# Kernel tuning notes

Measured on AMD Instinct MI355X. Metric: run time of the kernel, lower is better.

Reference implementation:

```python
import jax, jax.numpy as jnp
import numpy as np

N_NODES = 50000
N_EDGES = 800000
N_FEAT = 256
HIDDEN = 64
N_CLASSES = 16
T_END = 3.0  # opt['time']; rk4 takes one step over [0, 3]


def spline_conv(x, src, dst, p, W, R, b, n):
    """SplineConv, dim=1, kernel_size=2, degree=1 open B-spline, aggr='mean'.
    x: [n, Cin]; src/dst: [E]; p: [E,1] pseudo-coords in [0,1];
    W: [2, Cin, Cout]; R: [Cin, Cout]; b: [Cout]."""
    xj = x[src]  # gather source node features [E, Cin]
    # basis weights for K=2, degree=1: (1-p) on kernel 0, p on kernel 1
    msg = ((1.0 - p) * xj) @ W[0] + (p * xj) @ W[1]  # [E, Cout]
    agg = jax.ops.segment_sum(msg, dst, num_segments=n)
    deg = jax.ops.segment_sum(jnp.ones((msg.shape[0], 1), msg.dtype), dst, num_segments=n)
    return agg / jnp.maximum(deg, 1.0) + x @ R + b


def setup_inputs() -> dict:
    key = jax.random.key(0)
    ks = jax.random.split(key, 20)
    x = jax.random.normal(ks[0], (N_NODES, N_FEAT), jnp.float32)
    edge_attr = jax.random.uniform(ks[1], (N_EDGES, 1), jnp.float32)
    src = jax.random.randint(ks[2], (N_EDGES,), 0, N_NODES)
    dst = jax.random.randint(ks[3], (N_EDGES,), 0, N_NODES)

    def w(k, shape, fan_in):
        s = 1.0 / np.sqrt(fan_in)
        return jax.random.uniform(k, shape, jnp.float32, -s, s)

    # conv1: num_features -> hidden
    W1 = w(ks[4], (2, N_FEAT, HIDDEN), N_FEAT)
    R1 = w(ks[5], (N_FEAT, HIDDEN), N_FEAT)
    b1 = jnp.zeros((HIDDEN,), jnp.float32)
    # ODE func: two stacked SplineConvs hidden -> hidden
    Wa = w(ks[6], (2, HIDDEN, HIDDEN), HIDDEN)
    Ra = w(ks[7], (HIDDEN, HIDDEN), HIDDEN)
    ba = jnp.zeros((HIDDEN,), jnp.float32)
    Wb = w(ks[8], (2, HIDDEN, HIDDEN), HIDDEN)
    Rb = w(ks[9], (HIDDEN, HIDDEN), HIDDEN)
    bb = jnp.zeros((HIDDEN,), jnp.float32)
    # conv2: hidden -> num_classes
    W2 = w(ks[10], (2, HIDDEN, N_CLASSES), HIDDEN)
    R2 = w(ks[11], (HIDDEN, N_CLASSES), HIDDEN)
    b2 = jnp.zeros((N_CLASSES,), jnp.float32)

    return dict(x=x, edge_attr=edge_attr, src=src, dst=dst,
                W1=W1, R1=R1, b1=b1, Wa=Wa, Ra=Ra, ba=ba,
                Wb=Wb, Rb=Rb, bb=bb, W2=W2, R2=R2, b2=b2)


def reference(x, edge_attr, src, dst, W1, R1, b1, Wa, Ra, ba, Wb, Rb, bb, W2, R2, b2):
    n = x.shape[0]
    p = edge_attr
    h = jnp.tanh(spline_conv(x, src, dst, p, W1, R1, b1, n))
    # dropout is identity in eval mode

    def f(y):  # GCNLayer: two stacked SplineConvs, no activation
        y = spline_conv(y, src, dst, p, Wa, Ra, ba, n)
        return spline_conv(y, src, dst, p, Wb, Rb, bb, n)

    # single RK4 step from t=0 to t=T_END (torchdiffeq fixed-grid rk4 on s_span=[0,3])
    k1 = f(h)
    k2 = f(h + 0.5 * T_END * k1)
    k3 = f(h + 0.5 * T_END * k2)
    k4 = f(h + T_END * k3)
    h = h + (T_END / 6.0) * (k1 + 2.0 * k2 + 2.0 * k3 + k4)

    out = jnp.tanh(spline_conv(h, src, dst, p, W2, R2, b2, n))
    return jax.nn.log_softmax(out, axis=1)
```

## Files before the change

### kernel.cpp

```cpp
#include <hip/hip_runtime.h>
#include <math.h>

static inline int ceil_div(int a, int b) { return (a + b - 1) / b; }


__global__ __launch_bounds__(256) void zero2(int* __restrict__ a, int* __restrict__ b,
                                             int n) {
    int i = blockIdx.x * 256 + threadIdx.x;
    if (i < n) { a[i] = 0; b[i] = 0; }
}

__global__ __launch_bounds__(256) void hist_kernel(const int* __restrict__ dst,
                                                   int* __restrict__ deg, int E) {
    int e = blockIdx.x * 256 + threadIdx.x;
    if (e < E) atomicAdd(&deg[dst[e]], 1);
}

__global__ __launch_bounds__(256) void scan_blocksum(const int* __restrict__ deg,
                                                     int* __restrict__ bsum, int n) {
    __shared__ int red[256];
    int t = threadIdx.x;
    int base = blockIdx.x * 2048 + t * 8;
    int s = 0;
    #pragma unroll
    for (int i = 0; i < 8; ++i) {
        int idx = base + i;
        if (idx < n) s += deg[idx];
    }
    red[t] = s;
    __syncthreads();
    #pragma unroll
    for (int off = 128; off >= 1; off >>= 1) {
        if (t < off) red[t] += red[t + off];
        __syncthreads();
    }
    if (t == 0) bsum[blockIdx.x] = red[0];
}

__global__ __launch_bounds__(256) void scan_tops(int* __restrict__ bsum, int nb) {
    __shared__ int sh[256];
    int t = threadIdx.x;
    int orig = (t < nb) ? bsum[t] : 0;
    sh[t] = orig;
    __syncthreads();
    for (int off = 1; off < 256; off <<= 1) {
        int add = (t >= off) ? sh[t - off] : 0;
        __syncthreads();
        sh[t] += add;
        __syncthreads();
    }
    if (t < nb) bsum[t] = sh[t] - orig;
}

__global__ __launch_bounds__(256) void scan_final(const int* __restrict__ deg,
                                                  const int* __restrict__ bsum,
                                                  int* __restrict__ rowp,
                                                  float* __restrict__ invd,
                                                  int n, int E) {
    __shared__ int sh[256];
    int t = threadIdx.x;
    int base = blockIdx.x * 2048 + t * 8;
    int loc[8];
    int s = 0;
    #pragma unroll
    for (int i = 0; i < 8; ++i) {
        int idx = base + i;
        int d = (idx < n) ? deg[idx] : 0;
        loc[i] = d;
        s += d;
    }
    sh[t] = s;
    __syncthreads();
    for (int off = 1; off < 256; off <<= 1) {
        int add = (t >= off) ? sh[t - off] : 0;
        __syncthreads();
        sh[t] += add;
        __syncthreads();
    }
    int run = bsum[blockIdx.x] + (sh[t] - s);
    #pragma unroll
    for (int i = 0; i < 8; ++i) {
        int idx = base + i;
        if (idx < n) {
            rowp[idx] = run;
            int d = loc[i];
            run += d;
            invd[idx] = 1.0f / (float)(d > 1 ? d : 1);
        }
    }
    if (blockIdx.x == 0 && t == 0) rowp[n] = E;
}

__global__ __launch_bounds__(256) void scatter_idx(const int* __restrict__ dst,
                                                   const int* __restrict__ rowp,
                                                   int* __restrict__ fill,
                                                   int* __restrict__ ei, int E) {
    int e = blockIdx.x * 256 + threadIdx.x;
    if (e >= E) return;
    int d = dst[e];
    int pos = rowp[d] + atomicAdd(&fill[d], 1);
    ei[pos] = e;
}

__global__ __launch_bounds__(256) void sort_fill(const int* __restrict__ rowp,
                                                 int* __restrict__ ei,
                                                 const int* __restrict__ src,
                                                 const float* __restrict__ p,
                                                 int* __restrict__ es,
                                                 float* __restrict__ ep, int n) {
    int node = blockIdx.x * 256 + threadIdx.x;
    if (node >= n) return;
    int b = rowp[node], e = rowp[node + 1];
    for (int i = b + 1; i < e; ++i) {
        int key = ei[i];
        int j = i - 1;
        while (j >= b && ei[j] > key) { ei[j + 1] = ei[j]; --j; }
        ei[j + 1] = key;
    }
    for (int i = b; i < e; ++i) {
        int id = ei[i];
        es[i] = src[id];
        ep[i] = p[id];
    }
}

__global__ __launch_bounds__(256) void pack_all(
    const float* __restrict__ W1, const float* __restrict__ R1,
    const float* __restrict__ Wa, const float* __restrict__ Ra,
    const float* __restrict__ Wb, const float* __restrict__ Rb,
    const float* __restrict__ W2, const float* __restrict__ R2,
    float* __restrict__ Bc1, float* __restrict__ Bca,
    float* __restrict__ Bcb, float* __restrict__ Bc2) {
    int idx = blockIdx.x * 256 + threadIdx.x;
    const int S1 = 256 * 192, S2 = 192 * 64, S4 = 64 * 48;
    if (idx < S1) {
        int k = idx / 192, c = idx % 192;
        float v;
        if (c < 64)       v = W1[k * 64 + c];
        else if (c < 128) v = W1[256 * 64 + k * 64 + (c - 64)];
        else              v = R1[k * 64 + (c - 128)];
        Bc1[idx] = v;
        return;
    }
    idx -= S1;
    if (idx < S2) { Bca[idx] = (idx < 8192) ? Wa[idx] : Ra[idx - 8192]; return; }
    idx -= S2;
    if (idx < S2) { Bcb[idx] = (idx < 8192) ? Wb[idx] : Rb[idx - 8192]; return; }
    idx -= S2;
    if (idx < S4) {
        int k = idx / 48, c = idx % 48;
        float v;
        if (c < 16)      v = W2[k * 16 + c];
        else if (c < 32) v = W2[64 * 16 + k * 16 + (c - 16)];
        else             v = R2[k * 16 + (c - 32)];
        Bc2[idx] = v;
    }
}

__global__ __launch_bounds__(256) void edge_agg64_v4(const float* __restrict__ x,
                                                     const int* __restrict__ rowp,
                                                     const int* __restrict__ es,
                                                     const float* __restrict__ ep,
                                                     const float* __restrict__ invd,
                                                     float* __restrict__ agg, int n) {
    int gid = blockIdx.x * 256 + threadIdx.x;
    int node = gid >> 4;
    if (node >= n) return;
    int c4 = (gid & 15) << 2;
    int e = rowp[node], eend = rowp[node + 1];
    float sx = 0.f, sy = 0.f, sz = 0.f, sw = 0.f;
    float px = 0.f, py = 0.f, pz = 0.f, pw = 0.f;
    for (; e + 4 <= eend; e += 4) {
        int s0 = es[e], s1 = es[e + 1], s2 = es[e + 2], s3 = es[e + 3];
        float p0 = ep[e], p1 = ep[e + 1], p2 = ep[e + 2], p3 = ep[e + 3];
        float4 v0 = *reinterpret_cast<const float4*>(&x[(size_t)s0 * 64 + c4]);
        float4 v1 = *reinterpret_cast<const float4*>(&x[(size_t)s1 * 64 + c4]);
        float4 v2 = *reinterpret_cast<const float4*>(&x[(size_t)s2 * 64 + c4]);
        float4 v3 = *reinterpret_cast<const float4*>(&x[(size_t)s3 * 64 + c4]);
        sx += (v0.x + v1.x) + (v2.x + v3.x);
        sy += (v0.y + v1.y) + (v2.y + v3.y);
        sz += (v0.z + v1.z) + (v2.z + v3.z);
        sw += (v0.w + v1.w) + (v2.w + v3.w);
        px = fmaf(p0, v0.x, fmaf(p1, v1.x, fmaf(p2, v2.x, fmaf(p3, v3.x, px))));
        py = fmaf(p0, v0.y, fmaf(p1, v1.y, fmaf(p2, v2.y, fmaf(p3, v3.y, py))));
        pz = fmaf(p0, v0.z, fmaf(p1, v1.z, fmaf(p2, v2.z, fmaf(p3, v3.z, pz))));
        pw = fmaf(p0, v0.w, fmaf(p1, v1.w, fmaf(p2, v2.w, fmaf(p3, v3.w, pw))));
    }
    for (; e < eend; ++e) {
        int s = es[e];
        float pe = ep[e];
        float4 v = *reinterpret_cast<const float4*>(&x[(size_t)s * 64 + c4]);
        sx += v.x; sy += v.y; sz += v.z; sw += v.w;
        px = fmaf(pe, v.x, px); py = fmaf(pe, v.y, py);
        pz = fmaf(pe, v.z, pz); pw = fmaf(pe, v.w, pw);
    }
    float w = invd[node];
    float4 a0 = make_float4((sx - px) * w, (sy - py) * w, (sz - pz) * w, (sw - pw) * w);
    float4 a1 = make_float4(px * w, py * w, pz * w, pw * w);
    *reinterpret_cast<float4*>(&agg[(size_t)node * 128 + c4]) = a0;
    *reinterpret_cast<float4*>(&agg[(size_t)node * 128 + 64 + c4]) = a1;
}

__global__ __launch_bounds__(256) void hidden_gemm_db(
    const float* __restrict__ agg, const float* __restrict__ in,
    const float* __restrict__ B, const float* __restrict__ bias,
    int n, int mode, float* __restrict__ u_out,
    const float* __restrict__ hbuf, const float* __restrict__ acc_in,
    float* __restrict__ acc_out, float* __restrict__ t_out,
    float c1, float c2, float c3) {
    __shared__ __align__(16) float As[2][16][68];
    __shared__ __align__(16) float Bs[2][16][68];
    const int t = threadIdx.x;
    const int row0 = blockIdx.x * 64;
    const int ty = t >> 4, tx = t & 15;
    const int lrow = t >> 2, lk = (t & 3) << 2;
    const int bkk = t >> 4, bcol = (t & 15) << 2;

    float4 av = make_float4(0.f, 0.f, 0.f, 0.f);
    {
        int r = row0 + lrow;
        if (r < n) av = *reinterpret_cast<const float4*>(&agg[(size_t)r * 128 + lk]);
    }
    float4 bv = *reinterpret_cast<const float4*>(&B[(size_t)bkk * 64 + bcol]);
    As[0][lk + 0][lrow] = av.x; As[0][lk + 1][lrow] = av.y;
    As[0][lk + 2][lrow] = av.z; As[0][lk + 3][lrow] = av.w;
    *reinterpret_cast<float4*>(&Bs[0][bkk][bcol]) = bv;
    __syncthreads();

    float acc[4][4];
    #pragma unroll
    for (int i = 0; i < 4; ++i)
        #pragma unroll
        for (int j = 0; j < 4; ++j) acc[i][j] = 0.f;

    for (int kt = 0; kt < 12; ++kt) {
        const int cur = kt & 1;
        if (kt + 1 < 12) {
            int k0 = (kt + 1) << 4;
            int r = row0 + lrow;
            int kk = k0 + lk;
            av = make_float4(0.f, 0.f, 0.f, 0.f);
            if (r < n)
                av = (kk < 128)
                    ? *reinterpret_cast<const float4*>(&agg[(size_t)r * 128 + kk])
                    : *reinterpret_cast<const float4*>(&in[(size_t)r * 64 + (kk - 128)]);
            bv = *reinterpret_cast<const float4*>(&B[(size_t)(k0 + bkk) * 64 + bcol]);
        }
        #pragma unroll
        for (int kk = 0; kk < 16; ++kk) {
            float4 a4 = *reinterpret_cast<const float4*>(&As[cur][kk][ty << 2]);
            float4 b4 = *reinterpret_cast<const float4*>(&Bs[cur][kk][tx << 2]);
            float aa[4] = {a4.x, a4.y, a4.z, a4.w};
            float bb[4] = {b4.x, b4.y, b4.z, b4.w};
            #pragma unroll
            for (int i = 0; i < 4; ++i)
                #pragma unroll
                for (int j = 0; j < 4; ++j)
                    acc[i][j] = fmaf(aa[i], bb[j], acc[i][j]);
        }
        if (kt + 1 < 12) {
            const int nx = cur ^ 1;
            As[nx][lk + 0][lrow] = av.x; As[nx][lk + 1][lrow] = av.y;
            As[nx][lk + 2][lrow] = av.z; As[nx][lk + 3][lrow] = av.w;
            *reinterpret_cast<float4*>(&Bs[nx][bkk][bcol]) = bv;
        }
        __syncthreads();
    }

    float4 bia = *reinterpret_cast<const float4*>(&bias[tx << 2]);
    #pragma unroll
    for (int i = 0; i < 4; ++i) {
        int r = row0 + (ty << 2) + i;
        if (r >= n) continue;
        size_t idx = (size_t)r * 64 + (tx << 2);
        float4 v = make_float4(acc[i][0] + bia.x, acc[i][1] + bia.y,
                               acc[i][2] + bia.z, acc[i][3] + bia.w);
        if (mode == 0) {
            *reinterpret_cast<float4*>(&u_out[idx]) = v;
        } else {
            float4 ai = make_float4(0.f, 0.f, 0.f, 0.f);
            if (acc_in) ai = *reinterpret_cast<const float4*>(&acc_in[idx]);
            float4 an = make_float4(ai.x + c3 * v.x, ai.y + c3 * v.y,
                                    ai.z + c3 * v.z, ai.w + c3 * v.w);
            *reinterpret_cast<float4*>(&acc_out[idx]) = an;
            float4 hb = *reinterpret_cast<const float4*>(&hbuf[idx]);
            float4 to = make_float4(hb.x + c1 * v.x + c2 * an.x,
                                    hb.y + c1 * v.y + c2 * an.y,
                                    hb.z + c1 * v.z + c2 * an.z,
                                    hb.w + c1 * v.w + c2 * an.w);
            *reinterpret_cast<float4*>(&t_out[idx]) = to;
        }
    }
}

__global__ __launch_bounds__(256) void conv1_gemm_db(const float* __restrict__ x,
                                                     const float* __restrict__ B,
                                                     int n, float* __restrict__ yz,
                                                     float* __restrict__ base,
                                                     const float* __restrict__ b1) {
    __shared__ __align__(16) float As[2][16][68];
    __shared__ __align__(16) float Bs[2][16][200];
    const int t = threadIdx.x;
    const int row0 = blockIdx.x * 64;
    const int ty = t >> 4, tx = t & 15;
    const int lrow = t >> 2, lk = (t & 3) << 2;
    const int bkk = t >> 4, bcol = (t & 15) << 2;

    float4 av = make_float4(0.f, 0.f, 0.f, 0.f);
    {
        int r = row0 + lrow;
        if (r < n) av = *reinterpret_cast<const float4*>(&x[(size_t)r * 256 + lk]);
    }
    const float* bp0 = &B[(size_t)bkk * 192 + bcol];
    float4 bv0 = *reinterpret_cast<const float4*>(bp0);
    float4 bv1 = *reinterpret_cast<const float4*>(bp0 + 64);
    float4 bv2 = *reinterpret_cast<const float4*>(bp0 + 128);
    As[0][lk + 0][lrow] = av.x; As[0][lk + 1][lrow] = av.y;
    As[0][lk + 2][lrow] = av.z; As[0][lk + 3][lrow] = av.w;
    *reinterpret_cast<float4*>(&Bs[0][bkk][bcol]) = bv0;
    *reinterpret_cast<float4*>(&Bs[0][bkk][bcol + 64]) = bv1;
    *reinterpret_cast<float4*>(&Bs[0][bkk][bcol + 128]) = bv2;
    __syncthreads();

    float acc[4][12];
    #pragma unroll
    for (int i = 0; i < 4; ++i)
        #pragma unroll
        for (int j = 0; j < 12; ++j) acc[i][j] = 0.f;

    for (int kt = 0; kt < 16; ++kt) {
        const int cur = kt & 1;
        if (kt + 1 < 16) {
            int k0 = (kt + 1) << 4;
            int r = row0 + lrow;
            av = make_float4(0.f, 0.f, 0.f, 0.f);
            if (r < n)
                av = *reinterpret_cast<const float4*>(&x[(size_t)r * 256 + k0 + lk]);
            const float* bp = &B[(size_t)(k0 + bkk) * 192 + bcol];
            bv0 = *reinterpret_cast<const float4*>(bp);
            bv1 = *reinterpret_cast<const float4*>(bp + 64);
            bv2 = *reinterpret_cast<const float4*>(bp + 128);
        }
        #pragma unroll
        for (int kk = 0; kk < 16; ++kk) {
            float4 a4 = *reinterpret_cast<const float4*>(&As[cur][kk][ty << 2]);
            float4 b0 = *reinterpret_cast<const float4*>(&Bs[cur][kk][tx << 2]);
            float4 b1v = *reinterpret_cast<const float4*>(&Bs[cur][kk][(tx << 2) + 64]);
            float4 b2v = *reinterpret_cast<const float4*>(&Bs[cur][kk][(tx << 2) + 128]);
            float aa[4] = {a4.x, a4.y, a4.z, a4.w};
            float bb[12] = {b0.x, b0.y, b0.z, b0.w, b1v.x, b1v.y, b1v.z, b1v.w,
                            b2v.x, b2v.y, b2v.z, b2v.w};
            #pragma unroll
            for (int i = 0; i < 4; ++i)
                #pragma unroll
                for (int j = 0; j < 12; ++j)
                    acc[i][j] = fmaf(aa[i], bb[j], acc[i][j]);
        }
        if (kt + 1 < 16) {
            const int nx = cur ^ 1;
            As[nx][lk + 0][lrow] = av.x; As[nx][lk + 1][lrow] = av.y;
            As[nx][lk + 2][lrow] = av.z; As[nx][lk + 3][lrow] = av.w;
            *reinterpret_cast<float4*>(&Bs[nx][bkk][bcol]) = bv0;
            *reinterpret_cast<float4*>(&Bs[nx][bkk][bcol + 64]) = bv1;
            *reinterpret_cast<float4*>(&Bs[nx][bkk][bcol + 128]) = bv2;
        }
        __syncthreads();
    }

    float4 bb4 = *reinterpret_cast<const float4*>(&b1[tx << 2]);
    #pragma unroll
    for (int i = 0; i < 4; ++i) {
        int r = row0 + (ty << 2) + i;
        if (r >= n) continue;
        float4 q0 = make_float4(acc[i][0], acc[i][1], acc[i][2], acc[i][3]);
        float4 q1 = make_float4(acc[i][4], acc[i][5], acc[i][6], acc[i][7]);
        float4 q2 = make_float4(acc[i][8] + bb4.x, acc[i][9] + bb4.y,
                                acc[i][10] + bb4.z, acc[i][11] + bb4.w);
        *reinterpret_cast<float4*>(&yz[(size_t)r * 128 + (tx << 2)]) = q0;
        *reinterpret_cast<float4*>(&yz[(size_t)r * 128 + 64 + (tx << 2)]) = q1;
        *reinterpret_cast<float4*>(&base[(size_t)r * 64 + (tx << 2)]) = q2;
    }
}


__global__ __launch_bounds__(256) void edge_tf64_v4(const float* __restrict__ yz,
                                                    const int* __restrict__ rowp,
                                                    const int* __restrict__ es,
                                                    const float* __restrict__ ep,
                                                    const float* __restrict__ invd,
                                                    const float* __restrict__ base,
                                                    float* __restrict__ out, int n) {
    int gid = blockIdx.x * 256 + threadIdx.x;
    int node = gid >> 4;
    if (node >= n) return;
    int c4 = (gid & 15) << 2;
    int e = rowp[node], eend = rowp[node + 1];
    float ax = 0.f, ay = 0.f, az = 0.f, aw = 0.f;
    for (; e + 2 <= eend; e += 2) {
        int s0 = es[e], s1 = es[e + 1];
        float p0 = ep[e], p1 = ep[e + 1];
        float4 y0 = *reinterpret_cast<const float4*>(&yz[(size_t)s0 * 128 + c4]);
        float4 z0 = *reinterpret_cast<const float4*>(&yz[(size_t)s0 * 128 + 64 + c4]);
        float4 y1 = *reinterpret_cast<const float4*>(&yz[(size_t)s1 * 128 + c4]);
        float4 z1 = *reinterpret_cast<const float4*>(&yz[(size_t)s1 * 128 + 64 + c4]);
        ax += fmaf(p0, z0.x - y0.x, y0.x) + fmaf(p1, z1.x - y1.x, y1.x);
        ay += fmaf(p0, z0.y - y0.y, y0.y) + fmaf(p1, z1.y - y1.y, y1.y);
        az += fmaf(p0, z0.z - y0.z, y0.z) + fmaf(p1, z1.z - y1.z, y1.z);
        aw += fmaf(p0, z0.w - y0.w, y0.w) + fmaf(p1, z1.w - y1.w, y1.w);
    }
    for (; e < eend; ++e) {
        int s = es[e];
        float pe = ep[e];
        float4 y = *reinterpret_cast<const float4*>(&yz[(size_t)s * 128 + c4]);
        float4 z = *reinterpret_cast<const float4*>(&yz[(size_t)s * 128 + 64 + c4]);
        ax += fmaf(pe, z.x - y.x, y.x);
        ay += fmaf(pe, z.y - y.y, y.y);
        az += fmaf(pe, z.z - y.z, y.z);
        aw += fmaf(pe, z.w - y.w, y.w);
    }
    float w = invd[node];
    size_t idx = (size_t)node * 64 + c4;
    float4 b = *reinterpret_cast<const float4*>(&base[idx]);
    float4 o = make_float4(tanhf(fmaf(ax, w, b.x)), tanhf(fmaf(ay, w, b.y)),
                           tanhf(fmaf(az, w, b.z)), tanhf(fmaf(aw, w, b.w)));
    *reinterpret_cast<float4*>(&out[idx]) = o;
}

__global__ __launch_bounds__(256) void edge_tf16_lsm(const float* __restrict__ yz,
                                                     const int* __restrict__ rowp,
                                                     const int* __restrict__ es,
                                                     const float* __restrict__ ep,
                                                     const float* __restrict__ invd,
                                                     const float* __restrict__ base,
                                                     float* __restrict__ out, int n) {
    int gid = blockIdx.x * 256 + threadIdx.x;
    int node = gid >> 4;
    if (node >= n) return;
    int c = gid & 15;
    int e = rowp[node], eend = rowp[node + 1];
    float a = 0.f;
    for (; e + 4 <= eend; e += 4) {
        int s0 = es[e], s1 = es[e + 1], s2 = es[e + 2], s3 = es[e + 3];
        float p0 = ep[e], p1 = ep[e + 1], p2 = ep[e + 2], p3 = ep[e + 3];
        float y0 = yz[(size_t)s0 * 32 + c],      z0 = yz[(size_t)s0 * 32 + 16 + c];
        float y1 = yz[(size_t)s1 * 32 + c],      z1 = yz[(size_t)s1 * 32 + 16 + c];
        float y2 = yz[(size_t)s2 * 32 + c],      z2 = yz[(size_t)s2 * 32 + 16 + c];
        float y3 = yz[(size_t)s3 * 32 + c],      z3 = yz[(size_t)s3 * 32 + 16 + c];
        a += fmaf(p0, z0 - y0, y0);
        a += fmaf(p1, z1 - y1, y1);
        a += fmaf(p2, z2 - y2, y2);
        a += fmaf(p3, z3 - y3, y3);
    }
    for (; e < eend; ++e) {
        int s = es[e]; float pe = ep[e];
        float y = yz[(size_t)s * 32 + c], z = yz[(size_t)s * 32 + 16 + c];
        a += fmaf(pe, z - y, y);
    }
    float o = tanhf(a * invd[node] + base[(size_t)node * 16 + c]);
    float m = o;
    #pragma unroll
    for (int off = 8; off >= 1; off >>= 1) m = fmaxf(m, __shfl_xor(m, off, 16));
    float ex = expf(o - m);
    float s = ex;
    #pragma unroll
    for (int off = 8; off >= 1; off >>= 1) s += __shfl_xor(s, off, 16);
    out[(size_t)node * 16 + c] = (o - m) - logf(s);
}

__global__ __launch_bounds__(256) void gemm_tiled(
    const float* __restrict__ A0, int lda0, int K0,
    const float* __restrict__ A1, int lda1,
    const float* __restrict__ B,
    int n, int K, int M,
    float* __restrict__ out0, int w0, const float* __restrict__ bias0,
    float* __restrict__ out1, int w1, const float* __restrict__ bias1,
    int split) {
    __shared__ __align__(16) float As[16][68];
    __shared__ __align__(16) float Bs[16][68];
    const int t = threadIdx.x;
    const int row0 = blockIdx.x * 64;
    const int col0 = blockIdx.y * 64;
    const int ty = t >> 4, tx = t & 15;
    const int lrow = t >> 2, lk = (t & 3) << 2;
    const int bkk = t >> 4, bcol = (t & 15) << 2;
    float acc[4][4];
    #pragma unroll
    for (int i = 0; i < 4; ++i)
        #pragma unroll
        for (int j = 0; j < 4; ++j) acc[i][j] = 0.f;

    for (int k0 = 0; k0 < K; k0 += 16) {
        float4 av = make_float4(0.f, 0.f, 0.f, 0.f);
        {
            int r = row0 + lrow;
            if (r < n) {
                int kk = k0 + lk;
                const float* src = (kk < K0)
                    ? (A0 + (size_t)r * lda0 + kk)
                    : (A1 + (size_t)r * lda1 + (kk - K0));
                av = *reinterpret_cast<const float4*>(src);
            }
        }
        float4 bv = make_float4(0.f, 0.f, 0.f, 0.f);
        {
            int c = col0 + bcol;
            int kk = k0 + bkk;
            if (c < M) bv = *reinterpret_cast<const float4*>(B + (size_t)kk * M + c);
        }
        As[lk + 0][lrow] = av.x; As[lk + 1][lrow] = av.y;
        As[lk + 2][lrow] = av.z; As[lk + 3][lrow] = av.w;
        *reinterpret_cast<float4*>(&Bs[bkk][bcol]) = bv;
        __syncthreads();
        #pragma unroll
        for (int kk = 0; kk < 16; ++kk) {
            float4 a4 = *reinterpret_cast<const float4*>(&As[kk][ty << 2]);
            float4 b4 = *reinterpret_cast<const float4*>(&Bs[kk][tx << 2]);
            float aa[4] = {a4.x, a4.y, a4.z, a4.w};
            float bb[4] = {b4.x, b4.y, b4.z, b4.w};
            #pragma unroll
            for (int i = 0; i < 4; ++i)
                #pragma unroll
                for (int j = 0; j < 4; ++j)
                    acc[i][j] = fmaf(aa[i], bb[j], acc[i][j]);
        }
        __syncthreads();
    }

    #pragma unroll
    for (int i = 0; i < 4; ++i) {
        int r = row0 + (ty << 2) + i;
        if (r >= n) continue;
        #pragma unroll
        for (int j = 0; j < 4; ++j) {
            int c = col0 + (tx << 2) + j;
            if (c >= M) continue;
            float v = acc[i][j];
            if (c < split) {
                if (bias0) v += bias0[c];
                out0[(size_t)r * w0 + c] = v;
            } else {
                int cc = c - split;
                if (bias1) v += bias1[cc];
                out1[(size_t)r * w1 + cc] = v;
            }
        }
    }
}


static void hidden_conv(hipStream_t stream, const float* in, float* agg,
                        const int* rowp, const int* es, const float* ep,
                        const float* invd, const float* Bc, const float* bias, int n,
                        int mode, float* u_out,
                        const float* h, const float* acc_in, float* acc_out,
                        float* t_out, float c1, float c2, float c3) {
    edge_agg64_v4<<<ceil_div(n * 16, 256), 256, 0, stream>>>(in, rowp, es, ep, invd,
                                                             agg, n);
    hidden_gemm_db<<<ceil_div(n, 64), 256, 0, stream>>>(agg, in, Bc, bias, n, mode,
                                                        u_out, h, acc_in, acc_out,
                                                        t_out, c1, c2, c3);
}

extern "C" void kernel_launch(void* const* d_in, const int* in_sizes, int n_in,
                              void* d_out, int out_size, void* d_ws, size_t ws_size,
                              hipStream_t stream) {
    const float* x  = (const float*)d_in[0];
    const float* pE = (const float*)d_in[1];
    const int*   sr = (const int*)d_in[2];
    const int*   ds = (const int*)d_in[3];
    const float* W1 = (const float*)d_in[4];
    const float* R1 = (const float*)d_in[5];
    const float* b1 = (const float*)d_in[6];
    const float* Wa = (const float*)d_in[7];
    const float* Ra = (const float*)d_in[8];
    const float* ba = (const float*)d_in[9];
    const float* Wb = (const float*)d_in[10];
    const float* Rb = (const float*)d_in[11];
    const float* bb = (const float*)d_in[12];
    const float* W2 = (const float*)d_in[13];
    const float* R2 = (const float*)d_in[14];
    const float* b2 = (const float*)d_in[15];
    const int n = in_sizes[0] / 256;
    const int E = in_sizes[2];
    float* out = (float*)d_out;

    char* w = (char*)d_ws;
    auto alloc = [&](size_t bytes) -> void* {
        void* ptr = (void*)w;
        w += (bytes + 255) & ~(size_t)255;
        return ptr;
    };
    int nscan = ceil_div(n, 2048);
    int*   deg  = (int*)alloc((size_t)n * 4);
    int*   fill = (int*)alloc((size_t)n * 4);
    int*   rowp = (int*)alloc((size_t)(n + 1) * 4);
    float* invd = (float*)alloc((size_t)n * 4);
    int*   bsum = (int*)alloc((size_t)256 * 4);
    int*   ei   = (int*)alloc((size_t)E * 4);
    int*   es   = (int*)alloc((size_t)E * 4);
    float* ep   = (float*)alloc((size_t)E * 4);
    float* Bc1  = (float*)alloc((size_t)256 * 192 * 4);
    float* Bca  = (float*)alloc((size_t)192 * 64 * 4);
    float* Bcb  = (float*)alloc((size_t)192 * 64 * 4);
    float* Bc2  = (float*)alloc((size_t)64 * 48 * 4);
    float* big0 = (float*)alloc((size_t)n * 128 * 4);
    float* big1 = (float*)alloc((size_t)n * 64 * 4);
    float* h    = (float*)alloc((size_t)n * 64 * 4);
    float* u    = (float*)alloc((size_t)n * 64 * 4);
    float* tb   = (float*)alloc((size_t)n * 64 * 4);
    float* acc  = (float*)alloc((size_t)n * 64 * 4);

    const int PACK_TOTAL = 256 * 192 + 2 * 192 * 64 + 64 * 48;

    zero2<<<ceil_div(n, 256), 256, 0, stream>>>(deg, fill, n);
    pack_all<<<ceil_div(PACK_TOTAL, 256), 256, 0, stream>>>(W1, R1, Wa, Ra, Wb, Rb,
                                                            W2, R2, Bc1, Bca, Bcb, Bc2);
    hist_kernel<<<ceil_div(E, 256), 256, 0, stream>>>(ds, deg, E);
    scan_blocksum<<<nscan, 256, 0, stream>>>(deg, bsum, n);
    scan_tops<<<1, 256, 0, stream>>>(bsum, nscan);
    scan_final<<<nscan, 256, 0, stream>>>(deg, bsum, rowp, invd, n, E);
    scatter_idx<<<ceil_div(E, 256), 256, 0, stream>>>(ds, rowp, fill, ei, E);
    sort_fill<<<ceil_div(n, 256), 256, 0, stream>>>(rowp, ei, sr, pE, es, ep, n);

    const int gb = ceil_div(n, 64);

    conv1_gemm_db<<<gb, 256, 0, stream>>>(x, Bc1, n, big0, big1, b1);
    edge_tf64_v4<<<ceil_div(n * 16, 256), 256, 0, stream>>>(big0, rowp, es, ep, invd,
                                                            big1, h, n);

    hidden_conv(stream, h, big0, rowp, es, ep, invd, Bca, ba, n, 0, u,
                nullptr, nullptr, nullptr, nullptr, 0.f, 0.f, 0.f);
    hidden_conv(stream, u, big0, rowp, es, ep, invd, Bcb, bb, n, 1, nullptr,
                h, nullptr, acc, tb, 1.5f, 0.f, 1.f);
    hidden_conv(stream, tb, big0, rowp, es, ep, invd, Bca, ba, n, 0, u,
                nullptr, nullptr, nullptr, nullptr, 0.f, 0.f, 0.f);
    hidden_conv(stream, u, big0, rowp, es, ep, invd, Bcb, bb, n, 1, nullptr,
                h, acc, acc, tb, 1.5f, 0.f, 2.f);
    hidden_conv(stream, tb, big0, rowp, es, ep, invd, Bca, ba, n, 0, u,
                nullptr, nullptr, nullptr, nullptr, 0.f, 0.f, 0.f);
    hidden_conv(stream, u, big0, rowp, es, ep, invd, Bcb, bb, n, 1, nullptr,
                h, acc, acc, tb, 3.f, 0.f, 2.f);
    hidden_conv(stream, tb, big0, rowp, es, ep, invd, Bca, ba, n, 0, u,
                nullptr, nullptr, nullptr, nullptr, 0.f, 0.f, 0.f);
    hidden_conv(stream, u, big0, rowp, es, ep, invd, Bcb, bb, n, 1, nullptr,
                h, acc, acc, tb, 0.f, 0.5f, 1.f);

    gemm_tiled<<<dim3(gb, 1), 256, 0, stream>>>(tb, 64, 64, nullptr, 0, Bc2, n, 64, 48,
                                                big0, 32, nullptr, big1, 16, b2, 32);
    edge_tf16_lsm<<<ceil_div(n * 16, 256), 256, 0, stream>>>(big0, rowp, es, ep, invd,
                                                             big1, out, n);
}
```

Before: 926.0 us.

## Use 8-channel edge gathers and 32-row single-buffered GEMM tiles

The gather/aggregate kernels now give each thread 8 channels through two float4 loads, so 8 threads cover a node instead of 16. This halves the thread count and the index and weight loads per node, and adds more memory parallelism per thread. The hidden and conv1 GEMMs move from 64-row double-buffered tiles to 32-row single-buffered tiles, doubling the grid for better occupancy and cutting shared memory. The cost is lost load/compute overlap, half the threads idle during A-tile loads, and lower FMA reuse per thread.

```diff
diff --git a/kernel.cpp b/kernel.cpp
--- a/kernel.cpp
+++ b/kernel.cpp
@@ -157,120 +157,125 @@
     }
 }
 
-__global__ __launch_bounds__(256) void edge_agg64_v4(const float* __restrict__ x,
+__global__ __launch_bounds__(256) void edge_agg64_v8(const float* __restrict__ x,
                                                      const int* __restrict__ rowp,
                                                      const int* __restrict__ es,
                                                      const float* __restrict__ ep,
                                                      const float* __restrict__ invd,
                                                      float* __restrict__ agg, int n) {
     int gid = blockIdx.x * 256 + threadIdx.x;
-    int node = gid >> 4;
+    int node = gid >> 3;
     if (node >= n) return;
-    int c4 = (gid & 15) << 2;
+    int c8 = (gid & 7) << 3;
     int e = rowp[node], eend = rowp[node + 1];
-    float sx = 0.f, sy = 0.f, sz = 0.f, sw = 0.f;
-    float px = 0.f, py = 0.f, pz = 0.f, pw = 0.f;
+    float s[8] = {0.f, 0.f, 0.f, 0.f, 0.f, 0.f, 0.f, 0.f};
+    float p[8] = {0.f, 0.f, 0.f, 0.f, 0.f, 0.f, 0.f, 0.f};
     for (; e + 4 <= eend; e += 4) {
-        int s0 = es[e], s1 = es[e + 1], s2 = es[e + 2], s3 = es[e + 3];
+        int n0 = es[e], n1 = es[e + 1], n2 = es[e + 2], n3 = es[e + 3];
         float p0 = ep[e], p1 = ep[e + 1], p2 = ep[e + 2], p3 = ep[e + 3];
-        float4 v0 = *reinterpret_cast<const float4*>(&x[(size_t)s0 * 64 + c4]);
-        float4 v1 = *reinterpret_cast<const float4*>(&x[(size_t)s1 * 64 + c4]);
-        float4 v2 = *reinterpret_cast<const float4*>(&x[(size_t)s2 * 64 + c4]);
-        float4 v3 = *reinterpret_cast<const float4*>(&x[(size_t)s3 * 64 + c4]);
-        sx += (v0.x + v1.x) + (v2.x + v3.x);
-        sy += (v0.y + v1.y) + (v2.y + v3.y);
-        sz += (v0.z + v1.z) + (v2.z + v3.z);
-        sw += (v0.w + v1.w) + (v2.w + v3.w);
-        px = fmaf(p0, v0.x, fmaf(p1, v1.x, fmaf(p2, v2.x, fmaf(p3, v3.x, px))));
-        py = fmaf(p0, v0.y, fmaf(p1, v1.y, fmaf(p2, v2.y, fmaf(p3, v3.y, py))));
-        pz = fmaf(p0, v0.z, fmaf(p1, v1.z, fmaf(p2, v2.z, fmaf(p3, v3.z, pz))));
-        pw = fmaf(p0, v0.w, fmaf(p1, v1.w, fmaf(p2, v2.w, fmaf(p3, v3.w, pw))));
+        float4 v0a = *reinterpret_cast<const float4*>(&x[(size_t)n0 * 64 + c8]);
+        float4 v0b = *reinterpret_cast<const float4*>(&x[(size_t)n0 * 64 + c8 + 4]);
+        float4 v1a = *reinterpret_cast<const float4*>(&x[(size_t)n1 * 64 + c8]);
+        float4 v1b = *reinterpret_cast<const float4*>(&x[(size_t)n1 * 64 + c8 + 4]);
+        float4 v2a = *reinterpret_cast<const float4*>(&x[(size_t)n2 * 64 + c8]);
+        float4 v2b = *reinterpret_cast<const float4*>(&x[(size_t)n2 * 64 + c8 + 4]);
+        float4 v3a = *reinterpret_cast<const float4*>(&x[(size_t)n3 * 64 + c8]);
+        float4 v3b = *reinterpret_cast<const float4*>(&x[(size_t)n3 * 64 + c8 + 4]);
+        const float* f0 = &v0a.x; const float* f1 = &v1a.x;
+        const float* f2 = &v2a.x; const float* f3 = &v3a.x;
+        const float* g0 = &v0b.x; const float* g1 = &v1b.x;
+        const float* g2 = &v2b.x; const float* g3 = &v3b.x;
+        #pragma unroll
+        for (int j = 0; j < 4; ++j) {
+            s[j] += (f0[j] + f1[j]) + (f2[j] + f3[j]);
+            p[j] = fmaf(p0, f0[j], fmaf(p1, f1[j], fmaf(p2, f2[j], fmaf(p3, f3[j], p[j]))));
+        }
+        #pragma unroll
+        for (int j = 0; j < 4; ++j) {
+            s[4 + j] += (g0[j] + g1[j]) + (g2[j] + g3[j]);
+            p[4 + j] = fmaf(p0, g0[j], fmaf(p1, g1[j], fmaf(p2, g2[j], fmaf(p3, g3[j], p[4 + j]))));
+        }
     }
     for (; e < eend; ++e) {
-        int s = es[e];
+        int sn = es[e];
         float pe = ep[e];
-        float4 v = *reinterpret_cast<const float4*>(&x[(size_t)s * 64 + c4]);
-        sx += v.x; sy += v.y; sz += v.z; sw += v.w;
-        px = fmaf(pe, v.x, px); py = fmaf(pe, v.y, py);
-        pz = fmaf(pe, v.z, pz); pw = fmaf(pe, v.w, pw);
+        float4 va = *reinterpret_cast<const float4*>(&x[(size_t)sn * 64 + c8]);
+        float4 vb = *reinterpret_cast<const float4*>(&x[(size_t)sn * 64 + c8 + 4]);
+        const float* fa = &va.x; const float* fb = &vb.x;
+        #pragma unroll
+        for (int j = 0; j < 4; ++j) {
+            s[j] += fa[j];        p[j] = fmaf(pe, fa[j], p[j]);
+            s[4 + j] += fb[j];    p[4 + j] = fmaf(pe, fb[j], p[4 + j]);
+        }
     }
     float w = invd[node];
-    float4 a0 = make_float4((sx - px) * w, (sy - py) * w, (sz - pz) * w, (sw - pw) * w);
-    float4 a1 = make_float4(px * w, py * w, pz * w, pw * w);
-    *reinterpret_cast<float4*>(&agg[(size_t)node * 128 + c4]) = a0;
-    *reinterpret_cast<float4*>(&agg[(size_t)node * 128 + 64 + c4]) = a1;
-}
-
-__global__ __launch_bounds__(256) void hidden_gemm_db(
+    float4 a0, a1, b0, b1v;
+    a0.x = (s[0] - p[0]) * w; a0.y = (s[1] - p[1]) * w;
+    a0.z = (s[2] - p[2]) * w; a0.w = (s[3] - p[3]) * w;
+    a1.x = (s[4] - p[4]) * w; a1.y = (s[5] - p[5]) * w;
+    a1.z = (s[6] - p[6]) * w; a1.w = (s[7] - p[7]) * w;
+    b0.x = p[0] * w; b0.y = p[1] * w; b0.z = p[2] * w; b0.w = p[3] * w;
+    b1v.x = p[4] * w; b1v.y = p[5] * w; b1v.z = p[6] * w; b1v.w = p[7] * w;
+    *reinterpret_cast<float4*>(&agg[(size_t)node * 128 + c8])          = a0;
+    *reinterpret_cast<float4*>(&agg[(size_t)node * 128 + c8 + 4])      = a1;
+    *reinterpret_cast<float4*>(&agg[(size_t)node * 128 + 64 + c8])     = b0;
+    *reinterpret_cast<float4*>(&agg[(size_t)node * 128 + 64 + c8 + 4]) = b1v;
+}
+
+__global__ __launch_bounds__(256) void hidden_gemm32(
     const float* __restrict__ agg, const float* __restrict__ in,
     const float* __restrict__ B, const float* __restrict__ bias,
     int n, int mode, float* __restrict__ u_out,
     const float* __restrict__ hbuf, const float* __restrict__ acc_in,
     float* __restrict__ acc_out, float* __restrict__ t_out,
     float c1, float c2, float c3) {
-    __shared__ __align__(16) float As[2][16][68];
-    __shared__ __align__(16) float Bs[2][16][68];
+    __shared__ __align__(16) float As[16][36];
+    __shared__ __align__(16) float Bs[16][68];
     const int t = threadIdx.x;
-    const int row0 = blockIdx.x * 64;
+    const int row0 = blockIdx.x * 32;
     const int ty = t >> 4, tx = t & 15;
     const int lrow = t >> 2, lk = (t & 3) << 2;
     const int bkk = t >> 4, bcol = (t & 15) << 2;
-
-    float4 av = make_float4(0.f, 0.f, 0.f, 0.f);
-    {
-        int r = row0 + lrow;
-        if (r < n) av = *reinterpret_cast<const float4*>(&agg[(size_t)r * 128 + lk]);
-    }
-    float4 bv = *reinterpret_cast<const float4*>(&B[(size_t)bkk * 64 + bcol]);
-    As[0][lk + 0][lrow] = av.x; As[0][lk + 1][lrow] = av.y;
-    As[0][lk + 2][lrow] = av.z; As[0][lk + 3][lrow] = av.w;
-    *reinterpret_cast<float4*>(&Bs[0][bkk][bcol]) = bv;
-    __syncthreads();
-
-    float acc[4][4];
-    #pragma unroll
-    for (int i = 0; i < 4; ++i)
+    float acc[2][4];
+    #pragma unroll
+    for (int i = 0; i < 2; ++i)
         #pragma unroll
         for (int j = 0; j < 4; ++j) acc[i][j] = 0.f;
 
     for (int kt = 0; kt < 12; ++kt) {
-        const int cur = kt & 1;
-        if (kt + 1 < 12) {
-            int k0 = (kt + 1) << 4;
+        int k0 = kt << 4;
+        if (t < 128) {
             int r = row0 + lrow;
             int kk = k0 + lk;
-            av = make_float4(0.f, 0.f, 0.f, 0.f);
+            float4 av = make_float4(0.f, 0.f, 0.f, 0.f);
             if (r < n)
                 av = (kk < 128)
                     ? *reinterpret_cast<const float4*>(&agg[(size_t)r * 128 + kk])
                     : *reinterpret_cast<const float4*>(&in[(size_t)r * 64 + (kk - 128)]);
-            bv = *reinterpret_cast<const float4*>(&B[(size_t)(k0 + bkk) * 64 + bcol]);
-        }
+            As[lk + 0][lrow] = av.x; As[lk + 1][lrow] = av.y;
+            As[lk + 2][lrow] = av.z; As[lk + 3][lrow] = av.w;
+        }
+        float4 bv = *reinterpret_cast<const float4*>(&B[(size_t)(k0 + bkk) * 64 + bcol]);
+        *reinterpret_cast<float4*>(&Bs[bkk][bcol]) = bv;
+        __syncthreads();
         #pragma unroll
         for (int kk = 0; kk < 16; ++kk) {
-            float4 a4 = *reinterpret_cast<const float4*>(&As[cur][kk][ty << 2]);
-            float4 b4 = *reinterpret_cast<const float4*>(&Bs[cur][kk][tx << 2]);
-            float aa[4] = {a4.x, a4.y, a4.z, a4.w};
+            float a0 = As[kk][ty * 2], a1 = As[kk][ty * 2 + 1];
+            float4 b4 = *reinterpret_cast<const float4*>(&Bs[kk][tx << 2]);
             float bb[4] = {b4.x, b4.y, b4.z, b4.w};
             #pragma unroll
-            for (int i = 0; i < 4; ++i)
-                #pragma unroll
-                for (int j = 0; j < 4; ++j)
-                    acc[i][j] = fmaf(aa[i], bb[j], acc[i][j]);
-        }
-        if (kt + 1 < 12) {
-            const int nx = cur ^ 1;
-            As[nx][lk + 0][lrow] = av.x; As[nx][lk + 1][lrow] = av.y;
-            As[nx][lk + 2][lrow] = av.z; As[nx][lk + 3][lrow] = av.w;
-            *reinterpret_cast<float4*>(&Bs[nx][bkk][bcol]) = bv;
+            for (int j = 0; j < 4; ++j) {
+                acc[0][j] = fmaf(a0, bb[j], acc[0][j]);
+                acc[1][j] = fmaf(a1, bb[j], acc[1][j]);
+            }
         }
         __syncthreads();
     }
 
     float4 bia = *reinterpret_cast<const float4*>(&bias[tx << 2]);
     #pragma unroll
-    for (int i = 0; i < 4; ++i) {
-        int r = row0 + (ty << 2) + i;
+    for (int i = 0; i < 2; ++i) {
+        int r = row0 + ty * 2 + i;
         if (r >= n) continue;
         size_t idx = (size_t)r * 64 + (tx << 2);
         float4 v = make_float4(acc[i][0] + bia.x, acc[i][1] + bia.y,
@@ -293,84 +298,63 @@
     }
 }
 
-__global__ __launch_bounds__(256) void conv1_gemm_db(const float* __restrict__ x,
-                                                     const float* __restrict__ B,
-                                                     int n, float* __restrict__ yz,
-                                                     float* __restrict__ base,
-                                                     const float* __restrict__ b1) {
-    __shared__ __align__(16) float As[2][16][68];
-    __shared__ __align__(16) float Bs[2][16][200];
+__global__ __launch_bounds__(256) void conv1_gemm32(const float* __restrict__ x,
+                                                    const float* __restrict__ B,
+                                                    int n, float* __restrict__ yz,
+                                                    float* __restrict__ base,
+                                                    const float* __restrict__ b1) {
+    __shared__ __align__(16) float As[16][36];
+    __shared__ __align__(16) float Bs[16][200];
     const int t = threadIdx.x;
-    const int row0 = blockIdx.x * 64;
+    const int row0 = blockIdx.x * 32;
     const int ty = t >> 4, tx = t & 15;
     const int lrow = t >> 2, lk = (t & 3) << 2;
     const int bkk = t >> 4, bcol = (t & 15) << 2;
-
-    float4 av = make_float4(0.f, 0.f, 0.f, 0.f);
-    {
-        int r = row0 + lrow;
-        if (r < n) av = *reinterpret_cast<const float4*>(&x[(size_t)r * 256 + lk]);
-    }
-    const float* bp0 = &B[(size_t)bkk * 192 + bcol];
-    float4 bv0 = *reinterpret_cast<const float4*>(bp0);
-    float4 bv1 = *reinterpret_cast<const float4*>(bp0 + 64);
-    float4 bv2 = *reinterpret_cast<const float4*>(bp0 + 128);
-    As[0][lk + 0][lrow] = av.x; As[0][lk + 1][lrow] = av.y;
-    As[0][lk + 2][lrow] = av.z; As[0][lk + 3][lrow] = av.w;
-    *reinterpret_cast<float4*>(&Bs[0][bkk][bcol]) = bv0;
-    *reinterpret_cast<float4*>(&Bs[0][bkk][bcol + 64]) = bv1;
-    *reinterpret_cast<float4*>(&Bs[0][bkk][bcol + 128]) = bv2;
-    __syncthreads();
-
-    float acc[4][12];
-    #pragma unroll
-    for (int i = 0; i < 4; ++i)
+    float acc[2][12];
+    #pragma unroll
+    for (int i = 0; i < 2; ++i)
         #pragma unroll
         for (int j = 0; j < 12; ++j) acc[i][j] = 0.f;
 
     for (int kt = 0; kt < 16; ++kt) {
-        const int cur = kt & 1;
-        if (kt + 1 < 16) {
-            int k0 = (kt + 1) << 4;
+        int k0 = kt << 4;
+        if (t < 128) {
             int r = row0 + lrow;
-            av = make_float4(0.f, 0.f, 0.f, 0.f);
+            float4 av = make_float4(0.f, 0.f, 0.f, 0.f);
             if (r < n)
                 av = *reinterpret_cast<const float4*>(&x[(size_t)r * 256 + k0 + lk]);
-            const float* bp = &B[(size_t)(k0 + bkk) * 192 + bcol];
-            bv0 = *reinterpret_cast<const float4*>(bp);
-            bv1 = *reinterpret_cast<const float4*>(bp + 64);
-            bv2 = *reinterpret_cast<const float4*>(bp + 128);
-        }
+            As[lk + 0][lrow] = av.x; As[lk + 1][lrow] = av.y;
+            As[lk + 2][lrow] = av.z; As[lk + 3][lrow] = av.w;
+        }
+        const float* bp = &B[(size_t)(k0 + bkk) * 192 + bcol];
+        float4 bv0 = *reinterpret_cast<const float4*>(bp);
+        float4 bv1 = *reinterpret_cast<const float4*>(bp + 64);
+        float4 bv2 = *reinterpret_cast<const float4*>(bp + 128);
+        *reinterpret_cast<float4*>(&Bs[bkk][bcol])       = bv0;
+        *reinterpret_cast<float4*>(&Bs[bkk][bcol + 64])  = bv1;
+        *reinterpret_cast<float4*>(&Bs[bkk][bcol + 128]) = bv2;
+        __syncthreads();
         #pragma unroll
         for (int kk = 0; kk < 16; ++kk) {
-            float4 a4 = *reinterpret_cast<const float4*>(&As[cur][kk][ty << 2]);
-            float4 b0 = *reinterpret_cast<const float4*>(&Bs[cur][kk][tx << 2]);
-            float4 b1v = *reinterpret_cast<const float4*>(&Bs[cur][kk][(tx << 2) + 64]);
-            float4 b2v = *reinterpret_cast<const float4*>(&Bs[cur][kk][(tx << 2) + 128]);
-            float aa[4] = {a4.x, a4.y, a4.z, a4.w};
-            float bb[12] = {b0.x, b0.y, b0.z, b0.w, b1v.x, b1v.y, b1v.z, b1v.w,
-                            b2v.x, b2v.y, b2v.z, b2v.w};
+            float a0 = As[kk][ty * 2], a1 = As[kk][ty * 2 + 1];
+            float4 b0 = *reinterpret_cast<const float4*>(&Bs[kk][tx << 2]);
+            float4 b1q = *reinterpret_cast<const float4*>(&Bs[kk][(tx << 2) + 64]);
+            float4 b2q = *reinterpret_cast<const float4*>(&Bs[kk][(tx << 2) + 128]);
+            float bb[12] = {b0.x, b0.y, b0.z, b0.w, b1q.x, b1q.y, b1q.z, b1q.w,
+                            b2q.x, b2q.y, b2q.z, b2q.w};
             #pragma unroll
-            for (int i = 0; i < 4; ++i)
-                #pragma unroll
-                for (int j = 0; j < 12; ++j)
-                    acc[i][j] = fmaf(aa[i], bb[j], acc[i][j]);
-        }
-        if (kt + 1 < 16) {
-            const int nx = cur ^ 1;
-            As[nx][lk + 0][lrow] = av.x; As[nx][lk + 1][lrow] = av.y;
-            As[nx][lk + 2][lrow] = av.z; As[nx][lk + 3][lrow] = av.w;
-            *reinterpret_cast<float4*>(&Bs[nx][bkk][bcol]) = bv0;
-            *reinterpret_cast<float4*>(&Bs[nx][bkk][bcol + 64]) = bv1;
-            *reinterpret_cast<float4*>(&Bs[nx][bkk][bcol + 128]) = bv2;
+            for (int j = 0; j < 12; ++j) {
+                acc[0][j] = fmaf(a0, bb[j], acc[0][j]);
+                acc[1][j] = fmaf(a1, bb[j], acc[1][j]);
+            }
         }
         __syncthreads();
     }
 
     float4 bb4 = *reinterpret_cast<const float4*>(&b1[tx << 2]);
     #pragma unroll
-    for (int i = 0; i < 4; ++i) {
-        int r = row0 + (ty << 2) + i;
+    for (int i = 0; i < 2; ++i) {
+        int r = row0 + ty * 2 + i;
         if (r >= n) continue;
         float4 q0 = make_float4(acc[i][0], acc[i][1], acc[i][2], acc[i][3]);
         float4 q1 = make_float4(acc[i][4], acc[i][5], acc[i][6], acc[i][7]);
@@ -382,8 +366,7 @@
     }
 }
 
-
-__global__ __launch_bounds__(256) void edge_tf64_v4(const float* __restrict__ yz,
+__global__ __launch_bounds__(256) void edge_tf64_v8(const float* __restrict__ yz,
                                                     const int* __restrict__ rowp,
                                                     const int* __restrict__ es,
                                                     const float* __restrict__ ep,
@@ -391,39 +374,57 @@
                                                     const float* __restrict__ base,
                                                     float* __restrict__ out, int n) {
     int gid = blockIdx.x * 256 + threadIdx.x;
-    int node = gid >> 4;
+    int node = gid >> 3;
     if (node >= n) return;
-    int c4 = (gid & 15) << 2;
+    int c8 = (gid & 7) << 3;
     int e = rowp[node], eend = rowp[node + 1];
-    float ax = 0.f, ay = 0.f, az = 0.f, aw = 0.f;
+    float a[8] = {0.f, 0.f, 0.f, 0.f, 0.f, 0.f, 0.f, 0.f};
     for (; e + 2 <= eend; e += 2) {
         int s0 = es[e], s1 = es[e + 1];
         float p0 = ep[e], p1 = ep[e + 1];
-        float4 y0 = *reinterpret_cast<const float4*>(&yz[(size_t)s0 * 128 + c4]);
-        float4 z0 = *reinterpret_cast<const float4*>(&yz[(size_t)s0 * 128 + 64 + c4]);
-        float4 y1 = *reinterpret_cast<const float4*>(&yz[(size_t)s1 * 128 + c4]);
-        float4 z1 = *reinterpret_cast<const float4*>(&yz[(size_t)s1 * 128 + 64 + c4]);
-        ax += fmaf(p0, z0.x - y0.x, y0.x) + fmaf(p1, z1.x - y1.x, y1.x);
-        ay += fmaf(p0, z0.y - y0.y, y0.y) + fmaf(p1, z1.y - y1.y, y1.y);
-        az += fmaf(p0, z0.z - y0.z, y0.z) + fmaf(p1, z1.z - y1.z, y1.z);
-        aw += fmaf(p0, z0.w - y0.w, y0.w) + fmaf(p1, z1.w - y1.w, y1.w);
+        float4 y0a = *reinterpret_cast<const float4*>(&yz[(size_t)s0 * 128 + c8]);
+        float4 y0b = *reinterpret_cast<const float4*>(&yz[(size_t)s0 * 128 + c8 + 4]);
+        float4 z0a = *reinterpret_cast<const float4*>(&yz[(size_t)s0 * 128 + 64 + c8]);
+        float4 z0b = *reinterpret_cast<const float4*>(&yz[(size_t)s0 * 128 + 64 + c8 + 4]);
+        float4 y1a = *reinterpret_cast<const float4*>(&yz[(size_t)s1 * 128 + c8]);
+        float4 y1b = *reinterpret_cast<const float4*>(&yz[(size_t)s1 * 128 + c8 + 4]);
+        float4 z1a = *reinterpret_cast<const float4*>(&yz[(size_t)s1 * 128 + 64 + c8]);
+        float4 z1b = *reinterpret_cast<const float4*>(&yz[(size_t)s1 * 128 + 64 + c8 + 4]);
+        const float* ya0 = &y0a.x; const float* yb0 = &y0b.x;
+        const float* za0 = &z0a.x; const float* zb0 = &z0b.x;
+        const float* ya1 = &y1a.x; const float* yb1 = &y1b.x;
+        const float* za1 = &z1a.x; const float* zb1 = &z1b.x;
+        #pragma unroll
+        for (int j = 0; j < 4; ++j) {
+            a[j]     += fmaf(p0, za0[j] - ya0[j], ya0[j]) + fmaf(p1, za1[j] - ya1[j], ya1[j]);
+            a[4 + j] += fmaf(p0, zb0[j] - yb0[j], yb0[j]) + fmaf(p1, zb1[j] - yb1[j], yb1[j]);
+        }
     }
     for (; e < eend; ++e) {
         int s = es[e];
         float pe = ep[e];
-        float4 y = *reinterpret_cast<const float4*>(&yz[(size_t)s * 128 + c4]);
-        float4 z = *reinterpret_cast<const float4*>(&yz[(size_t)s * 128 + 64 + c4]);
-        ax += fmaf(pe, z.x - y.x, y.x);
-        ay += fmaf(pe, z.y - y.y, y.y);
-        az += fmaf(pe, z.z - y.z, y.z);
-        aw += fmaf(pe, z.w - y.w, y.w);
+        float4 ya = *reinterpret_cast<const float4*>(&yz[(size_t)s * 128 + c8]);
+        float4 yb = *reinterpret_cast<const float4*>(&yz[(size_t)s * 128 + c8 + 4]);
+        float4 za = *reinterpret_cast<const float4*>(&yz[(size_t)s * 128 + 64 + c8]);
+        float4 zb = *reinterpret_cast<const float4*>(&yz[(size_t)s * 128 + 64 + c8 + 4]);
+        const float* fy = &ya.x; const float* gy = &yb.x;
+        const float* fz = &za.x; const float* gz = &zb.x;
+        #pragma unroll
+        for (int j = 0; j < 4; ++j) {
+            a[j]     += fmaf(pe, fz[j] - fy[j], fy[j]);
+            a[4 + j] += fmaf(pe, gz[j] - gy[j], gy[j]);
+        }
     }
     float w = invd[node];
-    size_t idx = (size_t)node * 64 + c4;
-    float4 b = *reinterpret_cast<const float4*>(&base[idx]);
-    float4 o = make_float4(tanhf(fmaf(ax, w, b.x)), tanhf(fmaf(ay, w, b.y)),
-                           tanhf(fmaf(az, w, b.z)), tanhf(fmaf(aw, w, b.w)));
-    *reinterpret_cast<float4*>(&out[idx]) = o;
+    size_t idx = (size_t)node * 64 + c8;
+    float4 ba = *reinterpret_cast<const float4*>(&base[idx]);
+    float4 bbv = *reinterpret_cast<const float4*>(&base[idx + 4]);
+    float4 o0 = make_float4(tanhf(fmaf(a[0], w, ba.x)), tanhf(fmaf(a[1], w, ba.y)),
+                            tanhf(fmaf(a[2], w, ba.z)), tanhf(fmaf(a[3], w, ba.w)));
+    float4 o1 = make_float4(tanhf(fmaf(a[4], w, bbv.x)), tanhf(fmaf(a[5], w, bbv.y)),
+                            tanhf(fmaf(a[6], w, bbv.z)), tanhf(fmaf(a[7], w, bbv.w)));
+    *reinterpret_cast<float4*>(&out[idx]) = o0;
+    *reinterpret_cast<float4*>(&out[idx + 4]) = o1;
 }
 
 __global__ __launch_bounds__(256) void edge_tf16_lsm(const float* __restrict__ yz,
@@ -554,11 +555,11 @@
                         int mode, float* u_out,
                         const float* h, const float* acc_in, float* acc_out,
                         float* t_out, float c1, float c2, float c3) {
-    edge_agg64_v4<<<ceil_div(n * 16, 256), 256, 0, stream>>>(in, rowp, es, ep, invd,
-                                                             agg, n);
-    hidden_gemm_db<<<ceil_div(n, 64), 256, 0, stream>>>(agg, in, Bc, bias, n, mode,
-                                                        u_out, h, acc_in, acc_out,
-                                                        t_out, c1, c2, c3);
+    edge_agg64_v8<<<ceil_div(n * 8, 256), 256, 0, stream>>>(in, rowp, es, ep, invd,
+                                                            agg, n);
+    hidden_gemm32<<<ceil_div(n, 32), 256, 0, stream>>>(agg, in, Bc, bias, n, mode,
+                                                       u_out, h, acc_in, acc_out,
+                                                       t_out, c1, c2, c3);
 }
 
 extern "C" void kernel_launch(void* const* d_in, const int* in_sizes, int n_in,
@@ -622,11 +623,9 @@
     scatter_idx<<<ceil_div(E, 256), 256, 0, stream>>>(ds, rowp, fill, ei, E);
     sort_fill<<<ceil_div(n, 256), 256, 0, stream>>>(rowp, ei, sr, pE, es, ep, n);
 
-    const int gb = ceil_div(n, 64);
-
-    conv1_gemm_db<<<gb, 256, 0, stream>>>(x, Bc1, n, big0, big1, b1);
-    edge_tf64_v4<<<ceil_div(n * 16, 256), 256, 0, stream>>>(big0, rowp, es, ep, invd,
-                                                            big1, h, n);
+    conv1_gemm32<<<ceil_div(n, 32), 256, 0, stream>>>(x, Bc1, n, big0, big1, b1);
+    edge_tf64_v8<<<ceil_div(n * 8, 256), 256, 0, stream>>>(big0, rowp, es, ep, invd,
+                                                           big1, h, n);
 
     hidden_conv(stream, h, big0, rowp, es, ep, invd, Bca, ba, n, 0, u,
                 nullptr, nullptr, nullptr, nullptr, 0.f, 0.f, 0.f);
@@ -645,8 +644,9 @@
     hidden_conv(stream, u, big0, rowp, es, ep, invd, Bcb, bb, n, 1, nullptr,
                 h, acc, acc, tb, 0.f, 0.5f, 1.f);
 
-    gemm_tiled<<<dim3(gb, 1), 256, 0, stream>>>(tb, 64, 64, nullptr, 0, Bc2, n, 64, 48,
-                                                big0, 32, nullptr, big1, 16, b2, 32);
+    gemm_tiled<<<dim3(ceil_div(n, 64), 1), 256, 0, stream>>>(
+        tb, 64, 64, nullptr, 0, Bc2, n, 64, 48,
+        big0, 32, nullptr, big1, 16, b2, 32);
     edge_tf16_lsm<<<ceil_div(n * 16, 256), 256, 0, stream>>>(big0, rowp, es, ep, invd,
                                                              big1, out, n);
 }
```

Measured after the change: 933.1 us. About the same (+0.8%).
